# Kernel optimization log

Measured on AMD Instinct MI355X. Metric: run time of the kernel, lower is better.

Reference implementation:

```python
import jax, jax.numpy as jnp
import numpy as np

B, S, H, D = 2, 2048, 16, 64
HID = H * D


def setup_inputs() -> dict:
    key = jax.random.key(0)
    ks = jax.random.split(key, 9)
    s = 1.0 / np.sqrt(HID)
    return {
        "x": jax.random.normal(ks[0], (B, S, HID), dtype=jnp.float32),
        "Wq": jax.random.normal(ks[1], (HID, HID), dtype=jnp.float32) * s,
        "bq": jax.random.normal(ks[2], (HID,), dtype=jnp.float32) * s,
        "Wk": jax.random.normal(ks[3], (HID, HID), dtype=jnp.float32) * s,
        "bk": jax.random.normal(ks[4], (HID,), dtype=jnp.float32) * s,
        "Wv": jax.random.normal(ks[5], (HID, HID), dtype=jnp.float32) * s,
        "bv": jax.random.normal(ks[6], (HID,), dtype=jnp.float32) * s,
        "Wp": jax.random.normal(ks[7], (HID, HID), dtype=jnp.float32) * s,
        "bp": jax.random.normal(ks[8], (HID,), dtype=jnp.float32) * s,
    }


def reference(x, Wq, bq, Wk, bk, Wv, bv, Wp, bp):
    b, s, hid = x.shape
    d = hid // H
    # linear projections (torch Linear: x @ W.T + b), split heads -> [b, h, s, d]
    def heads(y):
        return y.reshape(b, s, H, d).transpose(0, 2, 1, 3)
    q = heads(x @ Wq.T + bq)
    k = heads(x @ Wk.T + bk)
    v = heads(x @ Wv.T + bv)
    scale = 1.0 / np.sqrt(d).astype(np.float32)
    att = jnp.einsum("bhqd,bhkd->bhqk", q, k) * scale
    causal = jnp.tril(jnp.ones((s, s), dtype=bool))  # [s, s]
    att = jnp.where(causal[None, None], att, -jnp.inf)
    att = jax.nn.softmax(att, axis=-1)
    y = jnp.einsum("bhqk,bhkd->bhqd", att, v)
    y = y.transpose(0, 2, 1, 3).reshape(b, s, hid)
    return y @ Wp.T + bp
```

## Files before the change

### kernel.cpp

```cpp
#include <hip/hip_runtime.h>


typedef unsigned short u16;
typedef float f32x4 __attribute__((ext_vector_type(4)));
typedef __bf16 bf16x8 __attribute__((ext_vector_type(8)));
typedef unsigned short u16x4 __attribute__((ext_vector_type(4)));
typedef unsigned short u16x8 __attribute__((ext_vector_type(8)));

constexpr int Bn = 2, SEQ = 2048, NH = 16, HD = 64, HID = 1024;
constexpr size_t NX = (size_t)Bn * SEQ * HID;
constexpr size_t NW = (size_t)HID * HID;

__device__ __forceinline__ u16 f2bf(float f) {
  unsigned u = __float_as_uint(f);
  u += 0x7fff + ((u >> 16) & 1);
  return (u16)(u >> 16);
}

__device__ __forceinline__ f32x4 mfma16(bf16x8 a, bf16x8 b, f32x4 c) {
  return __builtin_amdgcn_mfma_f32_16x16x32_bf16(a, b, c, 0, 0, 0);
}

__device__ __forceinline__ void gload16(const u16* g, u16* l) {
  __builtin_amdgcn_global_load_lds(
      (const __attribute__((address_space(1))) unsigned int*)(const void*)g,
      (__attribute__((address_space(3))) unsigned int*)(void*)l, 16, 0, 0);
}

__global__ void cvt_all(const float* __restrict__ x,
                        const float* __restrict__ Wq, const float* __restrict__ Wk,
                        const float* __restrict__ Wv, const float* __restrict__ Wp,
                        u16* __restrict__ xb, u16* __restrict__ wqb, u16* __restrict__ wkb,
                        u16* __restrict__ wvb, u16* __restrict__ wpb) {
  size_t i = ((size_t)blockIdx.x * blockDim.x + threadIdx.x) * 4;
  const float* s; u16* d; size_t off;
  if (i < NX) { s = x; d = xb; off = i; }
  else {
    size_t k = i - NX;
    int id = (int)(k >> 20);
    off = k & (NW - 1);
    s = (id == 0) ? Wq : (id == 1) ? Wk : (id == 2) ? Wv : Wp;
    d = (id == 0) ? wqb : (id == 1) ? wkb : (id == 2) ? wvb : wpb;
  }
  float4 v = *reinterpret_cast<const float4*>(s + off);
  u16x4 o = {f2bf(v.x), f2bf(v.y), f2bf(v.z), f2bf(v.w)};
  *reinterpret_cast<u16x4*>(d + off) = o;
}

__global__ __launch_bounds__(256) void qkv_gemm(
    const u16* __restrict__ A,
    const u16* __restrict__ W0, const u16* __restrict__ W1, const u16* __restrict__ W2,
    const float* __restrict__ b0, const float* __restrict__ b1, const float* __restrict__ b2,
    u16* __restrict__ out0, u16* __restrict__ out1, u16* __restrict__ out2)
{
  constexpr int K = HID;
  __shared__ u16 smem[16384];
  const int tid = threadIdx.x;
  const int lane = tid & 63, w = tid >> 6;
  const int wr = w >> 1, wc = w & 1;
  const int l15 = lane & 15, g = lane >> 4;
  const int m0 = blockIdx.y * 128;
  const int n0g = blockIdx.x * 128;
  const int id = n0g >> 10;
  const int n0 = n0g & (HID - 1);
  const u16* Bm = (id == 0) ? W0 : (id == 1) ? W1 : W2;
  const float* bias = (id == 0) ? b0 : (id == 1) ? b1 : b2;

  auto stage = [&](int buf, int kt) {
#pragma unroll
    for (int i = 0; i < 2; i++) {
      int chunk = tid + 256 * i;
      int r = chunk >> 2, c = (chunk & 3) << 3;
      gload16(&A[(size_t)(m0 + r) * K + kt + c], &smem[buf * 4096 + chunk * 8]);
      gload16(&Bm[(size_t)(n0 + r) * K + kt + c], &smem[8192 + buf * 4096 + chunk * 8]);
    }
  };

  f32x4 acc[4][4] = {};
  stage(0, 0);

  for (int ki = 0; ki < 32; ki++) {
    const int buf = ki & 1;
    __syncthreads();
    if (ki + 1 < 32) stage(buf ^ 1, (ki + 1) * 32);
    const u16* As = &smem[buf * 4096];
    const u16* Bs = &smem[8192 + buf * 4096];
    bf16x8 af[4], bfr[4];
#pragma unroll
    for (int mi = 0; mi < 4; mi++)
      af[mi] = *reinterpret_cast<const bf16x8*>(&As[(wr * 64 + mi * 16 + l15) * 32 + g * 8]);
#pragma unroll
    for (int ni = 0; ni < 4; ni++)
      bfr[ni] = *reinterpret_cast<const bf16x8*>(&Bs[(wc * 64 + ni * 16 + l15) * 32 + g * 8]);
#pragma unroll
    for (int mi = 0; mi < 4; mi++)
#pragma unroll
      for (int ni = 0; ni < 4; ni++)
        acc[mi][ni] = mfma16(af[mi], bfr[ni], acc[mi][ni]);
  }

  float bv[4];
#pragma unroll
  for (int ni = 0; ni < 4; ni++) bv[ni] = bias[n0 + wc * 64 + ni * 16 + l15];

  if (id == 2) {
    __syncthreads();
#pragma unroll
    for (int mi = 0; mi < 4; mi++)
#pragma unroll
      for (int ni = 0; ni < 4; ni++) {
        u16x4 pk;
#pragma unroll
        for (int r = 0; r < 4; r++) pk[r] = f2bf(acc[mi][ni][r] + bv[ni]);
        int d_loc = wc * 64 + ni * 16 + l15;
        int sq_base = wr * 64 + mi * 16 + g * 4;
        *reinterpret_cast<u16x4*>(
            &smem[d_loc * 128 + (sq_base ^ ((d_loc & 7) << 4))]) = pk;
      }
    __syncthreads();
    const int bb = m0 >> 11;
    const int sq0 = m0 & (SEQ - 1);
#pragma unroll
    for (int i = 0; i < 8; i++) {
      int chunk = tid + 256 * i;
      int d_loc = chunk >> 4;
      int sqc = (chunk & 15) << 3;
      u16x8 val = *reinterpret_cast<const u16x8*>(
          &smem[d_loc * 128 + (sqc ^ ((d_loc & 7) << 4))]);
      int gn = n0 + d_loc;
      int hh = gn >> 6, dd = gn & 63;
      *reinterpret_cast<u16x8*>(
          &out2[((size_t)(bb * NH + hh) * HD + dd) * SEQ + sq0 + sqc]) = val;
    }
  } else {
    u16* out = (id == 0) ? out0 : out1;
#pragma unroll
    for (int mi = 0; mi < 4; mi++)
#pragma unroll
      for (int ni = 0; ni < 4; ni++)
#pragma unroll
        for (int r = 0; r < 4; r++) {
          int gm = m0 + wr * 64 + mi * 16 + g * 4 + r;
          int gn = n0 + wc * 64 + ni * 16 + l15;
          int bb = gm >> 11, sq = gm & (SEQ - 1);
          int hh = gn >> 6, d = gn & 63;
          out[((size_t)(bb * NH + hh) * SEQ + sq) * HD + d] = f2bf(acc[mi][ni][r] + bv[ni]);
        }
  }
}

__global__ __launch_bounds__(256) void gemm_out(
    const u16* __restrict__ A, const u16* __restrict__ Bm,
    const float* __restrict__ bias, float* __restrict__ out)
{
  constexpr int K = HID, N = HID;
  __shared__ u16 As[2][64 * 32];
  __shared__ u16 Bs[2][128 * 32];
  const int tid = threadIdx.x;
  const int lane = tid & 63, w = tid >> 6;
  const int l15 = lane & 15, g = lane >> 4;
  const int m0 = blockIdx.y * 64, n0 = blockIdx.x * 128;

  auto stage = [&](int buf, int kt) {
    {
      int r = tid >> 2, c = (tid & 3) << 3;
      gload16(&A[(size_t)(m0 + r) * K + kt + c], &As[buf][tid * 8]);
    }
#pragma unroll
    for (int i = 0; i < 2; i++) {
      int chunk = tid + 256 * i;
      int r = chunk >> 2, c = (chunk & 3) << 3;
      gload16(&Bm[(size_t)(n0 + r) * K + kt + c], &Bs[buf][chunk * 8]);
    }
  };

  f32x4 acc[4][2] = {};
  stage(0, 0);

  for (int ki = 0; ki < 32; ki++) {
    const int buf = ki & 1;
    __syncthreads();
    if (ki + 1 < 32) stage(buf ^ 1, (ki + 1) * 32);
    bf16x8 af[4], bfr[2];
#pragma unroll
    for (int mi = 0; mi < 4; mi++)
      af[mi] = *reinterpret_cast<const bf16x8*>(&As[buf][(mi * 16 + l15) * 32 + g * 8]);
#pragma unroll
    for (int ni = 0; ni < 2; ni++)
      bfr[ni] = *reinterpret_cast<const bf16x8*>(&Bs[buf][(w * 32 + ni * 16 + l15) * 32 + g * 8]);
#pragma unroll
    for (int mi = 0; mi < 4; mi++)
#pragma unroll
      for (int ni = 0; ni < 2; ni++)
        acc[mi][ni] = mfma16(af[mi], bfr[ni], acc[mi][ni]);
  }

  float bv[2];
#pragma unroll
  for (int ni = 0; ni < 2; ni++) bv[ni] = bias[n0 + w * 32 + ni * 16 + l15];

#pragma unroll
  for (int mi = 0; mi < 4; mi++)
#pragma unroll
    for (int ni = 0; ni < 2; ni++)
#pragma unroll
      for (int r = 0; r < 4; r++) {
        int gm = m0 + mi * 16 + g * 4 + r;
        int gn = n0 + w * 32 + ni * 16 + l15;
        out[(size_t)gm * N + gn] = acc[mi][ni][r] + bv[ni];
      }
}

__global__ __launch_bounds__(256) void attn_kernel(
    const u16* __restrict__ Q, const u16* __restrict__ Kt,
    const u16* __restrict__ Vt, u16* __restrict__ Y)
{
  __shared__ u16 smK[3][4096];
  __shared__ u16 smV[3][4096];
  const int tid = threadIdx.x;
  const int lane = tid & 63, w = tid >> 6;
  const int l15 = lane & 15, g = lane >> 4;
  const int bid = blockIdx.x;
  const int xcd = bid & 7, kk = bid >> 3;
  const int bh = xcd * 4 + (kk >> 4);
  const int jb = kk & 15;
  const int b = bh >> 4, h = bh & 15;
  const int xs = l15 & 7;

  const size_t bhs = (size_t)bh;
  const u16* Qp = Q + bhs * SEQ * HD;
  const u16* Kp = Kt + bhs * SEQ * HD;
  const u16* Vp = Vt + bhs * HD * SEQ;

  int srow[2], sslot[2];
#pragma unroll
  for (int it = 0; it < 2; it++) {
    int idx = it * 256 + tid;
    srow[it] = idx >> 3;
    sslot[it] = (idx & 7) ^ (srow[it] & 7);
  }
  auto stage = [&](int buf, int kt) {
#pragma unroll
    for (int it = 0; it < 2; it++) {
      int idx = it * 256 + tid;
      gload16(Kp + (size_t)(kt + srow[it]) * HD + sslot[it] * 8, &smK[buf][idx * 8]);
      gload16(Vp + (size_t)srow[it] * SEQ + kt + sslot[it] * 8, &smV[buf][idx * 8]);
    }
  };

  const float QSC = 0.125f * 1.44269504088896f;
  const float NEG = -__builtin_inff();

  for (int pi = 0; pi < 2; pi++) {
    const int tile = pi ? (31 - jb) : jb;
    const int nt = tile + 1;
    const int q0 = tile * 64 + w * 16;
    const int qg = q0 + l15;

    __syncthreads();

    bf16x8 tq0 = *reinterpret_cast<const bf16x8*>(Qp + (size_t)qg * HD + g * 8);
    bf16x8 tq1 = *reinterpret_cast<const bf16x8*>(Qp + (size_t)qg * HD + 32 + g * 8);

    stage(0, 0);
    if (nt > 1) stage(1, 64);

    bf16x8 qf[2];
#pragma unroll
    for (int jj = 0; jj < 8; jj++) {
      qf[0][jj] = (__bf16)((float)tq0[jj] * QSC);
      qf[1][jj] = (__bf16)((float)tq1[jj] * QSC);
    }

    float m_run = NEG, l_run = 0.0f;
    f32x4 o[4] = {};

    for (int t = 0; t < nt; t++) {
      const int kt = t * 64;
      const u16* K_ = smK[t % 3];
      const u16* V_ = smV[t % 3];
      if (t + 1 < nt) { asm volatile("s_waitcnt vmcnt(4)" ::: "memory"); }
      else            { asm volatile("s_waitcnt vmcnt(0)" ::: "memory"); }
      __builtin_amdgcn_s_barrier();
      if (t + 2 < nt) stage((t + 2) % 3, kt + 128);

      f32x4 sa[4];
#pragma unroll
      for (int sub = 0; sub < 4; sub++) {
        int row = sub * 16 + l15;
        bf16x8 k0 = *reinterpret_cast<const bf16x8*>(&K_[row * 64 + ((0 + g) ^ xs) * 8]);
        bf16x8 k1 = *reinterpret_cast<const bf16x8*>(&K_[row * 64 + ((4 + g) ^ xs) * 8]);
        f32x4 a = {0.f, 0.f, 0.f, 0.f};
        a = mfma16(k0, qf[0], a);
        a = mfma16(k1, qf[1], a);
        sa[sub] = a;
      }

      float p[16];
      if (t == nt - 1) {
#pragma unroll
        for (int sub = 0; sub < 4; sub++)
#pragma unroll
          for (int r = 0; r < 4; r++) {
            int key = kt + sub * 16 + g * 4 + r;
            p[sub * 4 + r] = (key <= qg) ? sa[sub][r] : NEG;
          }
      } else {
#pragma unroll
        for (int sub = 0; sub < 4; sub++)
#pragma unroll
          for (int r = 0; r < 4; r++) p[sub * 4 + r] = sa[sub][r];
      }

      float t8[8], t4[4];
#pragma unroll
      for (int i = 0; i < 8; i++) t8[i] = fmaxf(p[i], p[i + 8]);
#pragma unroll
      for (int i = 0; i < 4; i++) t4[i] = fmaxf(t8[i], t8[i + 4]);
      float tmax = fmaxf(fmaxf(t4[0], t4[2]), fmaxf(t4[1], t4[3]));
      tmax = fmaxf(tmax, __shfl_xor(tmax, 16));
      tmax = fmaxf(tmax, __shfl_xor(tmax, 32));

      if (__any(tmax > m_run + 11.0f)) {
        float mnew = fmaxf(m_run, tmax);
        float fs = __builtin_amdgcn_exp2f(m_run - mnew);
        l_run *= fs;
#pragma unroll
        for (int db = 0; db < 4; db++) o[db] *= fs;
        m_run = mnew;
      }

      float pe[16];
      float s4[4] = {0.f, 0.f, 0.f, 0.f};
#pragma unroll
      for (int i = 0; i < 16; i++) {
        pe[i] = __builtin_amdgcn_exp2f(p[i] - m_run);
        s4[i & 3] += pe[i];
      }
      float psum = (s4[0] + s4[1]) + (s4[2] + s4[3]);
      psum += __shfl_xor(psum, 16);
      psum += __shfl_xor(psum, 32);
      l_run += psum;

#pragma unroll
      for (int half = 0; half < 2; half++) {
        bf16x8 pb;
#pragma unroll
        for (int jj = 0; jj < 8; jj++) pb[jj] = (__bf16)pe[8 * half + jj];
        const int s0 = ((4 * half + (g >> 1)) ^ xs) * 8 + 4 * (g & 1);
        const int s1 = ((4 * half + 2 + (g >> 1)) ^ xs) * 8 + 4 * (g & 1);
#pragma unroll
        for (int db = 0; db < 4; db++) {
          int vbase = (db * 16 + l15) * 64;
          u16x4 v0 = *reinterpret_cast<const u16x4*>(&V_[vbase + s0]);
          u16x4 v1 = *reinterpret_cast<const u16x4*>(&V_[vbase + s1]);
          u16x8 vau;
#pragma unroll
          for (int jj = 0; jj < 4; jj++) { vau[jj] = v0[jj]; vau[jj + 4] = v1[jj]; }
          bf16x8 va = __builtin_bit_cast(bf16x8, vau);
          o[db] = mfma16(va, pb, o[db]);
        }
      }
    }

    float rl = 1.0f / l_run;
#pragma unroll
    for (int db = 0; db < 4; db++) {
      u16x4 yo;
#pragma unroll
      for (int r = 0; r < 4; r++) yo[r] = f2bf(o[db][r] * rl);
      *reinterpret_cast<u16x4*>(
          Y + ((size_t)(b * SEQ) + qg) * HID + h * HD + db * 16 + g * 4) = yo;
    }
  }
}

extern "C" void kernel_launch(void* const* d_in, const int* in_sizes, int n_in,
                              void* d_out, int out_size, void* d_ws, size_t ws_size,
                              hipStream_t stream) {
  const float* x  = (const float*)d_in[0];
  const float* Wq = (const float*)d_in[1];
  const float* bq = (const float*)d_in[2];
  const float* Wk = (const float*)d_in[3];
  const float* bk = (const float*)d_in[4];
  const float* Wv = (const float*)d_in[5];
  const float* bv = (const float*)d_in[6];
  const float* Wp = (const float*)d_in[7];
  const float* bp = (const float*)d_in[8];

  u16* ws = (u16*)d_ws;
  u16* xb  = ws; ws += NX;
  u16* wqb = ws; ws += NW;
  u16* wkb = ws; ws += NW;
  u16* wvb = ws; ws += NW;
  u16* wpb = ws; ws += NW;
  u16* Qb  = ws; ws += NX;
  u16* Kb  = ws; ws += NX;
  u16* Vtb = ws; ws += NX;
  u16* Yb  = ws; ws += NX;

  const unsigned cvtBlocks = (unsigned)((NX + 4 * NW) / 4 / 256);
  cvt_all<<<cvtBlocks, 256, 0, stream>>>(x, Wq, Wk, Wv, Wp, xb, wqb, wkb, wvb, wpb);

  qkv_gemm<<<dim3(24, 32), 256, 0, stream>>>(xb, wqb, wkb, wvb, bq, bk, bv, Qb, Kb, Vtb);

  attn_kernel<<<dim3(512), 256, 0, stream>>>(Qb, Kb, Vtb, Yb);

  gemm_out<<<dim3(8, 64), 256, 0, stream>>>(Yb, wpb, bp, (float*)d_out);
}
```

Before: 118.9 us.

## Split attention into one query tile per block with quartile-ordered scheduling

The attention kernel now launches 1024 blocks that each handle a single 64-row query tile, instead of 512 blocks each processing a short and a long tile in sequence. Block IDs are mapped so tiles are issued in four quartile waves (longest first within alternating orders) with a fixed head-to-XCD mapping. The K/V shared-memory ring drops from triple to double buffering, with a barrier each iteration, and launch bounds request 4 blocks per CU for occupancy. The aim is better load balance and occupancy from more, smaller blocks. The cost is shallower prefetch and an extra barrier per iteration.

```diff
diff --git a/kernel.cpp b/kernel.cpp
--- a/kernel.cpp
+++ b/kernel.cpp
@@ -211,21 +211,33 @@
       }
 }
 
-__global__ __launch_bounds__(256) void attn_kernel(
+__global__ __launch_bounds__(256, 4) void attn_kernel(
     const u16* __restrict__ Q, const u16* __restrict__ Kt,
     const u16* __restrict__ Vt, u16* __restrict__ Y)
 {
-  __shared__ u16 smK[3][4096];
-  __shared__ u16 smV[3][4096];
+  __shared__ u16 smK[2][4096];
+  __shared__ u16 smV[2][4096];
   const int tid = threadIdx.x;
   const int lane = tid & 63, w = tid >> 6;
   const int l15 = lane & 15, g = lane >> 4;
   const int bid = blockIdx.x;
-  const int xcd = bid & 7, kk = bid >> 3;
-  const int bh = xcd * 4 + (kk >> 4);
-  const int jb = kk & 15;
+  const int q = bid >> 8;
+  const int rr = bid & 255;
+  const int xcd = rr & 7;
+  const int cu = (rr >> 3) & 31;
+  const int bh = xcd * 4 + (cu & 3);
+  const int s = cu >> 2;
+  int tile;
+  if (q == 0) tile = 24 + s;
+  else if (q == 1) tile = 23 - s;
+  else if (q == 2) tile = 8 + s;
+  else tile = 7 - s;
   const int b = bh >> 4, h = bh & 15;
   const int xs = l15 & 7;
+
+  const int nt = tile + 1;
+  const int q0 = tile * 64 + w * 16;
+  const int qg = q0 + l15;
 
   const size_t bhs = (size_t)bh;
   const u16* Qp = Q + bhs * SEQ * HD;
@@ -251,127 +263,115 @@
   const float QSC = 0.125f * 1.44269504088896f;
   const float NEG = -__builtin_inff();
 
-  for (int pi = 0; pi < 2; pi++) {
-    const int tile = pi ? (31 - jb) : jb;
-    const int nt = tile + 1;
-    const int q0 = tile * 64 + w * 16;
-    const int qg = q0 + l15;
-
+  bf16x8 tq0 = *reinterpret_cast<const bf16x8*>(Qp + (size_t)qg * HD + g * 8);
+  bf16x8 tq1 = *reinterpret_cast<const bf16x8*>(Qp + (size_t)qg * HD + 32 + g * 8);
+  stage(0, 0);
+  bf16x8 qf[2];
+#pragma unroll
+  for (int jj = 0; jj < 8; jj++) {
+    qf[0][jj] = (__bf16)((float)tq0[jj] * QSC);
+    qf[1][jj] = (__bf16)((float)tq1[jj] * QSC);
+  }
+
+  float m_run = NEG, l_run = 0.0f;
+  f32x4 o[4] = {};
+
+  for (int t = 0; t < nt; t++) {
+    const int kt = t * 64;
+    const int buf = t & 1;
     __syncthreads();
-
-    bf16x8 tq0 = *reinterpret_cast<const bf16x8*>(Qp + (size_t)qg * HD + g * 8);
-    bf16x8 tq1 = *reinterpret_cast<const bf16x8*>(Qp + (size_t)qg * HD + 32 + g * 8);
-
-    stage(0, 0);
-    if (nt > 1) stage(1, 64);
-
-    bf16x8 qf[2];
-#pragma unroll
-    for (int jj = 0; jj < 8; jj++) {
-      qf[0][jj] = (__bf16)((float)tq0[jj] * QSC);
-      qf[1][jj] = (__bf16)((float)tq1[jj] * QSC);
-    }
-
-    float m_run = NEG, l_run = 0.0f;
-    f32x4 o[4] = {};
-
-    for (int t = 0; t < nt; t++) {
-      const int kt = t * 64;
-      const u16* K_ = smK[t % 3];
-      const u16* V_ = smV[t % 3];
-      if (t + 1 < nt) { asm volatile("s_waitcnt vmcnt(4)" ::: "memory"); }
-      else            { asm volatile("s_waitcnt vmcnt(0)" ::: "memory"); }
-      __builtin_amdgcn_s_barrier();
-      if (t + 2 < nt) stage((t + 2) % 3, kt + 128);
-
-      f32x4 sa[4];
-#pragma unroll
-      for (int sub = 0; sub < 4; sub++) {
-        int row = sub * 16 + l15;
-        bf16x8 k0 = *reinterpret_cast<const bf16x8*>(&K_[row * 64 + ((0 + g) ^ xs) * 8]);
-        bf16x8 k1 = *reinterpret_cast<const bf16x8*>(&K_[row * 64 + ((4 + g) ^ xs) * 8]);
-        f32x4 a = {0.f, 0.f, 0.f, 0.f};
-        a = mfma16(k0, qf[0], a);
-        a = mfma16(k1, qf[1], a);
-        sa[sub] = a;
+    if (t + 1 < nt) stage(buf ^ 1, kt + 64);
+    const u16* K_ = smK[buf];
+    const u16* V_ = smV[buf];
+
+    f32x4 sa[4];
+#pragma unroll
+    for (int sub = 0; sub < 4; sub++) {
+      int row = sub * 16 + l15;
+      bf16x8 k0 = *reinterpret_cast<const bf16x8*>(&K_[row * 64 + ((0 + g) ^ xs) * 8]);
+      bf16x8 k1 = *reinterpret_cast<const bf16x8*>(&K_[row * 64 + ((4 + g) ^ xs) * 8]);
+      f32x4 a = {0.f, 0.f, 0.f, 0.f};
+      a = mfma16(k0, qf[0], a);
+      a = mfma16(k1, qf[1], a);
+      sa[sub] = a;
+    }
+
+    float p[16];
+    if (t == nt - 1) {
+#pragma unroll
+      for (int sub = 0; sub < 4; sub++)
+#pragma unroll
+        for (int r = 0; r < 4; r++) {
+          int key = kt + sub * 16 + g * 4 + r;
+          p[sub * 4 + r] = (key <= qg) ? sa[sub][r] : NEG;
+        }
+    } else {
+#pragma unroll
+      for (int sub = 0; sub < 4; sub++)
+#pragma unroll
+        for (int r = 0; r < 4; r++) p[sub * 4 + r] = sa[sub][r];
+    }
+
+    float a0 = fmaxf(fmaxf(p[0], p[1]), p[2]);
+    float a1 = fmaxf(fmaxf(p[3], p[4]), p[5]);
+    float a2 = fmaxf(fmaxf(p[6], p[7]), p[8]);
+    float a3 = fmaxf(fmaxf(p[9], p[10]), p[11]);
+    float a4 = fmaxf(fmaxf(p[12], p[13]), p[14]);
+    float b0 = fmaxf(fmaxf(a0, a1), p[15]);
+    float tmax = fmaxf(fmaxf(b0, a2), fmaxf(a3, a4));
+    tmax = fmaxf(tmax, __shfl_xor(tmax, 16));
+    tmax = fmaxf(tmax, __shfl_xor(tmax, 32));
+
+    if (__any(tmax > m_run + 11.0f)) {
+      float mnew = fmaxf(m_run, tmax);
+      float fs = __builtin_amdgcn_exp2f(m_run - mnew);
+      l_run *= fs;
+#pragma unroll
+      for (int db = 0; db < 4; db++) o[db] *= fs;
+      m_run = mnew;
+    }
+
+    float pe[16];
+    float s4[4] = {0.f, 0.f, 0.f, 0.f};
+#pragma unroll
+    for (int i = 0; i < 16; i++) {
+      pe[i] = __builtin_amdgcn_exp2f(p[i] - m_run);
+      s4[i & 3] += pe[i];
+    }
+    float psum = (s4[0] + s4[1]) + (s4[2] + s4[3]);
+    psum += __shfl_xor(psum, 16);
+    psum += __shfl_xor(psum, 32);
+    l_run += psum;
+
+#pragma unroll
+    for (int half = 0; half < 2; half++) {
+      bf16x8 pb;
+#pragma unroll
+      for (int jj = 0; jj < 8; jj++) pb[jj] = (__bf16)pe[8 * half + jj];
+      const int s0 = ((4 * half + (g >> 1)) ^ xs) * 8 + 4 * (g & 1);
+      const int s1 = ((4 * half + 2 + (g >> 1)) ^ xs) * 8 + 4 * (g & 1);
+#pragma unroll
+      for (int db = 0; db < 4; db++) {
+        int vbase = (db * 16 + l15) * 64;
+        u16x4 v0 = *reinterpret_cast<const u16x4*>(&V_[vbase + s0]);
+        u16x4 v1 = *reinterpret_cast<const u16x4*>(&V_[vbase + s1]);
+        u16x8 vau;
+#pragma unroll
+        for (int jj = 0; jj < 4; jj++) { vau[jj] = v0[jj]; vau[jj + 4] = v1[jj]; }
+        bf16x8 va = __builtin_bit_cast(bf16x8, vau);
+        o[db] = mfma16(va, pb, o[db]);
       }
-
-      float p[16];
-      if (t == nt - 1) {
-#pragma unroll
-        for (int sub = 0; sub < 4; sub++)
-#pragma unroll
-          for (int r = 0; r < 4; r++) {
-            int key = kt + sub * 16 + g * 4 + r;
-            p[sub * 4 + r] = (key <= qg) ? sa[sub][r] : NEG;
-          }
-      } else {
-#pragma unroll
-        for (int sub = 0; sub < 4; sub++)
-#pragma unroll
-          for (int r = 0; r < 4; r++) p[sub * 4 + r] = sa[sub][r];
-      }
-
-      float t8[8], t4[4];
-#pragma unroll
-      for (int i = 0; i < 8; i++) t8[i] = fmaxf(p[i], p[i + 8]);
-#pragma unroll
-      for (int i = 0; i < 4; i++) t4[i] = fmaxf(t8[i], t8[i + 4]);
-      float tmax = fmaxf(fmaxf(t4[0], t4[2]), fmaxf(t4[1], t4[3]));
-      tmax = fmaxf(tmax, __shfl_xor(tmax, 16));
-      tmax = fmaxf(tmax, __shfl_xor(tmax, 32));
-
-      if (__any(tmax > m_run + 11.0f)) {
-        float mnew = fmaxf(m_run, tmax);
-        float fs = __builtin_amdgcn_exp2f(m_run - mnew);
-        l_run *= fs;
-#pragma unroll
-        for (int db = 0; db < 4; db++) o[db] *= fs;
-        m_run = mnew;
-      }
-
-      float pe[16];
-      float s4[4] = {0.f, 0.f, 0.f, 0.f};
-#pragma unroll
-      for (int i = 0; i < 16; i++) {
-        pe[i] = __builtin_amdgcn_exp2f(p[i] - m_run);
-        s4[i & 3] += pe[i];
-      }
-      float psum = (s4[0] + s4[1]) + (s4[2] + s4[3]);
-      psum += __shfl_xor(psum, 16);
-      psum += __shfl_xor(psum, 32);
-      l_run += psum;
-
-#pragma unroll
-      for (int half = 0; half < 2; half++) {
-        bf16x8 pb;
-#pragma unroll
-        for (int jj = 0; jj < 8; jj++) pb[jj] = (__bf16)pe[8 * half + jj];
-        const int s0 = ((4 * half + (g >> 1)) ^ xs) * 8 + 4 * (g & 1);
-        const int s1 = ((4 * half + 2 + (g >> 1)) ^ xs) * 8 + 4 * (g & 1);
-#pragma unroll
-        for (int db = 0; db < 4; db++) {
-          int vbase = (db * 16 + l15) * 64;
-          u16x4 v0 = *reinterpret_cast<const u16x4*>(&V_[vbase + s0]);
-          u16x4 v1 = *reinterpret_cast<const u16x4*>(&V_[vbase + s1]);
-          u16x8 vau;
-#pragma unroll
-          for (int jj = 0; jj < 4; jj++) { vau[jj] = v0[jj]; vau[jj + 4] = v1[jj]; }
-          bf16x8 va = __builtin_bit_cast(bf16x8, vau);
-          o[db] = mfma16(va, pb, o[db]);
-        }
-      }
-    }
-
-    float rl = 1.0f / l_run;
-#pragma unroll
-    for (int db = 0; db < 4; db++) {
-      u16x4 yo;
-#pragma unroll
-      for (int r = 0; r < 4; r++) yo[r] = f2bf(o[db][r] * rl);
-      *reinterpret_cast<u16x4*>(
-          Y + ((size_t)(b * SEQ) + qg) * HID + h * HD + db * 16 + g * 4) = yo;
-    }
+    }
+  }
+
+  float rl = 1.0f / l_run;
+#pragma unroll
+  for (int db = 0; db < 4; db++) {
+    u16x4 yo;
+#pragma unroll
+    for (int r = 0; r < 4; r++) yo[r] = f2bf(o[db][r] * rl);
+    *reinterpret_cast<u16x4*>(
+        Y + ((size_t)(b * SEQ) + qg) * HID + h * HD + db * 16 + g * 4) = yo;
   }
 }
 
@@ -404,7 +404,7 @@
 
   qkv_gemm<<<dim3(24, 32), 256, 0, stream>>>(xb, wqb, wkb, wvb, bq, bk, bv, Qb, Kb, Vtb);
 
-  attn_kernel<<<dim3(512), 256, 0, stream>>>(Qb, Kb, Vtb, Yb);
+  attn_kernel<<<dim3(1024), 256, 0, stream>>>(Qb, Kb, Vtb, Yb);
 
   gemm_out<<<dim3(8, 64), 256, 0, stream>>>(Yb, wpb, bp, (float*)d_out);
 }
```

Result: faster. 114.5 us (-3.8%).
